# Performance work log

Measured on AMD Instinct MI355X. Metric: run time of the kernel, lower is better.

Reference implementation:

```python
import jax, jax.numpy as jnp
import numpy as np

RES = 32            # input grid resolution
OUT_RES = 64        # after subdivide
C = 128             # channels (== out_channels -> skip is identity)
G = 32              # group-norm groups
N = 8192            # active input voxels
EPS = 1e-5

# 8 child offsets for subdivide, 27 stencil offsets for 3x3x3 submanifold conv
_OFFS8 = np.stack(np.meshgrid([0, 1], [0, 1], [0, 1], indexing='ij'), -1).reshape(-1, 3).astype(np.int32)
_OFFS27 = np.stack(np.meshgrid([-1, 0, 1], [-1, 0, 1], [-1, 0, 1], indexing='ij'), -1).reshape(-1, 3).astype(np.int32)


def group_norm(x, gamma, beta, num_groups=G, eps=EPS):
    # sparse group norm over all active voxels of the (single) sample
    n, c = x.shape
    xg = x.reshape(n, num_groups, c // num_groups)
    mean = xg.mean(axis=(0, 2), keepdims=True)
    var = xg.var(axis=(0, 2), keepdims=True)
    xn = (xg - mean) * jax.lax.rsqrt(var + eps)
    return xn.reshape(n, c) * gamma + beta


def subdivide_coords(coords):
    offs = jnp.asarray(_OFFS8)
    return (coords[:, None, :] * 2 + offs[None, :, :]).reshape(-1, 3)  # [8N, 3]


def subm_conv3d(feats, coords, W, b, grid_res):
    # submanifold 3x3x3 sparse conv: outputs only at active sites
    n = feats.shape[0]
    grid = jnp.full((grid_res, grid_res, grid_res), -1, dtype=jnp.int32)
    grid = grid.at[coords[:, 0], coords[:, 1], coords[:, 2]].set(
        jnp.arange(n, dtype=jnp.int32))
    out = jnp.zeros((n, W.shape[-1]), dtype=feats.dtype)
    for k in range(27):  # fixed small stencil loop
        off = jnp.asarray(_OFFS27[k])
        nb = coords + off
        inb = jnp.all((nb >= 0) & (nb < grid_res), axis=1)
        nbc = jnp.clip(nb, 0, grid_res - 1)
        idx = grid[nbc[:, 0], nbc[:, 1], nbc[:, 2]]
        mask = inb & (idx >= 0)
        g = jnp.where(mask[:, None], feats[jnp.where(mask, idx, 0)], 0.0)
        out = out + g @ W[k]
    return out + b


def setup_inputs() -> dict:
    key = jax.random.key(0)
    ks = jax.random.split(key, 8)
    rng = np.random.default_rng(0)
    flat = rng.choice(RES ** 3, size=N, replace=False)
    coords = np.stack([flat // (RES * RES), (flat // RES) % RES, flat % RES],
                      axis=-1).astype(np.int32)
    feats = jax.random.normal(ks[0], (N, C), dtype=jnp.float32)
    gamma1 = 1.0 + 0.1 * jax.random.normal(ks[1], (C,), dtype=jnp.float32)
    beta1 = 0.1 * jax.random.normal(ks[2], (C,), dtype=jnp.float32)
    W1 = jax.random.normal(ks[3], (27, C, C), dtype=jnp.float32) * 0.05
    b1 = jax.random.normal(ks[4], (C,), dtype=jnp.float32) * 0.05
    gamma2 = 1.0 + 0.1 * jax.random.normal(ks[5], (C,), dtype=jnp.float32)
    beta2 = 0.1 * jax.random.normal(ks[6], (C,), dtype=jnp.float32)
    W2 = jax.random.normal(ks[7], (27, C, C), dtype=jnp.float32) * 0.05
    b2 = jax.random.normal(jax.random.fold_in(key, 99), (C,), dtype=jnp.float32) * 0.05
    return {"feats": feats, "gamma1": gamma1, "beta1": beta1, "W1": W1,
            "b1": b1, "gamma2": gamma2, "beta2": beta2, "W2": W2, "b2": b2,
            "coords": jnp.asarray(coords)}


def reference(feats, gamma1, beta1, W1, b1, gamma2, beta2, W2, b2, coords):
    # act_layers: GroupNorm + SiLU at input resolution
    h = jax.nn.silu(group_norm(feats, gamma1, beta1))
    # subdivide both branch and residual (8 children per voxel)
    new_coords = subdivide_coords(coords)          # [8N, 3] in OUT_RES grid
    h = jnp.repeat(h, 8, axis=0)
    x_sub = jnp.repeat(feats, 8, axis=0)
    # out_layers: conv3 -> GN -> SiLU -> conv3 (submanifold, same active set)
    h = subm_conv3d(h, new_coords, W1, b1, OUT_RES)
    h = jax.nn.silu(group_norm(h, gamma2, beta2))
    h = subm_conv3d(h, new_coords, W2, b2, OUT_RES)
    # skip_connection is Identity since out_channels == channels
    return h + x_sub
```

## Files before the change

### kernel.cpp

```cpp
#include <hip/hip_runtime.h>

#define NPAR   8192
#define NCH    65536
#define RES    32
#define EPS    1e-5f

typedef __attribute__((ext_vector_type(8))) short short8;
typedef __attribute__((ext_vector_type(4))) float floatx4;

__device__ __forceinline__ unsigned short f2bf(float f) {
    union { float f; unsigned u; } v; v.f = f;
    unsigned r = v.u + 0x7fffu + ((v.u >> 16) & 1u);
    return (unsigned short)(r >> 16);
}
__device__ __forceinline__ float bf2f(unsigned short b) {
    union { unsigned u; float f; } v; v.u = ((unsigned)b) << 16;
    return v.f;
}
__device__ __forceinline__ void glds16(const void* g, void* l) {
    __builtin_amdgcn_global_load_lds(
        (__attribute__((address_space(1))) const void*)g,
        (__attribute__((address_space(3))) void*)l, 16, 0, 0);
}
__device__ __forceinline__ int k27_of(int o, int s) {
    return (((o >> 2) & 1) + ((s >> 2) & 1)) * 9 +
           (((o >> 1) & 1) + ((s >> 1) & 1)) * 3 +
           ((o & 1) + (s & 1));
}
__device__ __forceinline__ void axis_dlist(int o, int s, int* d, int& n) {
    if (o == 0) { if (s == 0) { d[0] = -1; n = 1; } else { d[0] = 0; d[1] = 1; n = 2; } }
    else        { if (s == 0) { d[0] = -1; d[1] = 0; n = 2; } else { d[0] = 1; n = 1; } }
}

__global__ void k1_kernel(const int* __restrict__ coords, int* __restrict__ grid32,
                          const float* __restrict__ x, float* __restrict__ sum,
                          float* __restrict__ sq) {
    int b = blockIdx.x;
    int t = threadIdx.x;
    if (b < 32) {
        int p = b * 256 + t;
        grid32[(coords[p*3] << 10) + (coords[p*3+1] << 5) + coords[p*3+2]] = p;
    } else {
        __shared__ float s_sum[32], s_sq[32];
        if (t < 32) { s_sum[t] = 0.0f; s_sq[t] = 0.0f; }
        __syncthreads();
        const float4* x4 = (const float4*)x;
        int total = NPAR * 32;
        int idx0 = (b - 32) * 256 + t;
        int g = idx0 & 31;
        float ls = 0.0f, lq = 0.0f;
        for (int idx = idx0; idx < total; idx += 256 * 256) {
            float4 v = x4[idx];
            ls += v.x + v.y + v.z + v.w;
            lq += v.x * v.x + v.y * v.y + v.z * v.z + v.w * v.w;
        }
        atomicAdd(&s_sum[g], ls);
        atomicAdd(&s_sq[g], lq);
        __syncthreads();
        if (t < 32) { atomicAdd(&sum[t], s_sum[t]); atomicAdd(&sq[t], s_sq[t]); }
    }
}

__global__ void k2_kernel(const int* __restrict__ coords, const int* __restrict__ grid32,
                          int* __restrict__ idx_tab, int* __restrict__ pidx27,
                          const float* __restrict__ W1, const float* __restrict__ W2,
                          unsigned short* __restrict__ Wc1f, unsigned short* __restrict__ Wp2,
                          const float* __restrict__ x, const float* __restrict__ sum,
                          const float* __restrict__ sq, const float* __restrict__ gamma,
                          const float* __restrict__ beta, unsigned short* __restrict__ y) {
    int b = blockIdx.x;
    if (b < 256) {
        int R = b * 256 + threadIdx.x;
        int p = R >> 3, o = R & 7;
        int bx = 2 * coords[p*3]   + ((o >> 2) & 1);
        int by = 2 * coords[p*3+1] + ((o >> 1) & 1);
        int bz = 2 * coords[p*3+2] + (o & 1);
#pragma unroll 1
        for (int k = 0; k < 27; ++k) {
            int fx = bx + k / 9 - 1, fy = by + (k / 3) % 3 - 1, fz = bz + k % 3 - 1;
            int src = -1;
            if ((unsigned)fx < 64u && (unsigned)fy < 64u && (unsigned)fz < 64u) {
                int r = grid32[((fx >> 1) << 10) + ((fy >> 1) << 5) + (fz >> 1)];
                if ((unsigned)r < (unsigned)NPAR)
                    src = (((fx & 1) << 2) + ((fy & 1) << 1) + (fz & 1)) * NPAR + r;
            }
            idx_tab[k * NCH + R] = src;
        }
    } else if (b < 472) {
        int rem = (b - 256) * 256 + threadIdx.x;
        int lane = rem & 63;
        int ks   = (rem >> 6) & 3;
        int nb   = (rem >> 8) & 7;
        int tap  = rem >> 11;
        int n  = nb * 16 + (lane & 15);
        int k0 = ks * 32 + (lane >> 4) * 8;
        unsigned short v[8];
#pragma unroll
        for (int j = 0; j < 8; ++j) v[j] = f2bf(W2[tap * 16384 + (k0 + j) * 128 + n]);
        uint4 pk;
        pk.x = (unsigned)v[0] | ((unsigned)v[1] << 16);
        pk.y = (unsigned)v[2] | ((unsigned)v[3] << 16);
        pk.z = (unsigned)v[4] | ((unsigned)v[5] << 16);
        pk.w = (unsigned)v[6] | ((unsigned)v[7] << 16);
        *(uint4*)&Wp2[(long)rem * 8] = pk;
    } else if (b < 984) {
        int rem = (b - 472) * 256 + threadIdx.x;
        int lane  = rem & 63;
        int ks    = (rem >> 6) & 3;
        int nb    = (rem >> 8) & 7;
        int combo = rem >> 11;
        int o = combo >> 3, s = combo & 7;
        int n  = nb * 16 + (lane & 15);
        int k0 = ks * 32 + (lane >> 4) * 8;
        int d0[2], d1[2], d2[2], n0, n1, n2;
        axis_dlist((o >> 2) & 1, (s >> 2) & 1, d0, n0);
        axis_dlist((o >> 1) & 1, (s >> 1) & 1, d1, n1);
        axis_dlist(o & 1,        s & 1,        d2, n2);
        unsigned short v[8];
#pragma unroll
        for (int j = 0; j < 8; ++j) {
            float acc = 0.0f;
            for (int a = 0; a < n0; ++a)
                for (int bb = 0; bb < n1; ++bb)
                    for (int cc = 0; cc < n2; ++cc) {
                        int kk = (d0[a] + 1) * 9 + (d1[bb] + 1) * 3 + (d2[cc] + 1);
                        acc += W1[kk * 16384 + (k0 + j) * 128 + n];
                    }
            v[j] = f2bf(acc);
        }
        uint4 pk;
        pk.x = (unsigned)v[0] | ((unsigned)v[1] << 16);
        pk.y = (unsigned)v[2] | ((unsigned)v[3] << 16);
        pk.z = (unsigned)v[4] | ((unsigned)v[5] << 16);
        pk.w = (unsigned)v[6] | ((unsigned)v[7] << 16);
        *(uint4*)&Wc1f[(long)rem * 8] = pk;
    } else if (b < 1848) {
        int gid = (b - 984) * 256 + threadIdx.x;
        int k = gid >> 13, p = gid & 8191;
        int nx = coords[p*3]   + k / 9 - 1;
        int ny = coords[p*3+1] + (k / 3) % 3 - 1;
        int nz = coords[p*3+2] + k % 3 - 1;
        int src = -1;
        if ((unsigned)nx < 32u && (unsigned)ny < 32u && (unsigned)nz < 32u) {
            int r = grid32[(nx << 10) + (ny << 5) + nz];
            if ((unsigned)r < (unsigned)NPAR) src = r;
        }
        pidx27[k * NPAR + p] = src;
    } else {
        const float4* x4 = (const float4*)x;
        uint2* y2 = (uint2*)y;
        const float4* g4 = (const float4*)gamma;
        const float4* b4 = (const float4*)beta;
        float cnt = (float)NPAR * 4.0f;
        int total = NPAR * 32;
        for (int idx = (b - 1848) * 256 + threadIdx.x; idx < total; idx += 256 * 256) {
            int c4 = idx & 31;
            float mean = sum[c4] / cnt;
            float var = sq[c4] / cnt - mean * mean;
            float rstd = rsqrtf(var + EPS);
            float4 v = x4[idx];
            float4 gm = g4[c4];
            float4 bt = b4[c4];
            float a[4] = {v.x, v.y, v.z, v.w};
            float gg[4] = {gm.x, gm.y, gm.z, gm.w};
            float bb[4] = {bt.x, bt.y, bt.z, bt.w};
            unsigned short o[4];
#pragma unroll
            for (int i = 0; i < 4; ++i) {
                float tv = (a[i] - mean) * rstd * gg[i] + bb[i];
                o[i] = f2bf(tv / (1.0f + __expf(-tv)));
            }
            uint2 pk;
            pk.x = (unsigned)o[0] | ((unsigned)o[1] << 16);
            pk.y = (unsigned)o[2] | ((unsigned)o[3] << 16);
            y2[idx] = pk;
        }
    }
}

__global__ void gn_apply_bf16_kernel(unsigned short* __restrict__ x,
                                     const float* __restrict__ sum, const float* __restrict__ sq,
                                     const float* __restrict__ gamma, const float* __restrict__ beta,
                                     int nrows) {
    uint2* x2 = (uint2*)x;
    const float4* g4 = (const float4*)gamma;
    const float4* b4 = (const float4*)beta;
    float cnt = (float)nrows * 4.0f;
    int total = nrows * 32;
    for (int idx = blockIdx.x * blockDim.x + threadIdx.x; idx < total;
         idx += gridDim.x * blockDim.x) {
        int c4 = idx & 31;
        float mean = sum[c4] / cnt;
        float var = sq[c4] / cnt - mean * mean;
        float rstd = rsqrtf(var + EPS);
        uint2 pk = x2[idx];
        float a[4] = {bf2f((unsigned short)(pk.x & 0xffff)), bf2f((unsigned short)(pk.x >> 16)),
                      bf2f((unsigned short)(pk.y & 0xffff)), bf2f((unsigned short)(pk.y >> 16))};
        float4 gm = g4[c4];
        float4 bt = b4[c4];
        float gg[4] = {gm.x, gm.y, gm.z, gm.w};
        float bb[4] = {bt.x, bt.y, bt.z, bt.w};
        unsigned short o[4];
#pragma unroll
        for (int i = 0; i < 4; ++i) {
            float tv = (a[i] - mean) * rstd * gg[i] + bb[i];
            o[i] = f2bf(tv / (1.0f + __expf(-tv)));
        }
        pk.x = (unsigned)o[0] | ((unsigned)o[1] << 16);
        pk.y = (unsigned)o[2] | ((unsigned)o[3] << 16);
        x2[idx] = pk;
    }
}

__global__ void __launch_bounds__(256) conv1_fold_kernel(
    const unsigned short* __restrict__ Ag, const unsigned short* __restrict__ Wc1f,
    const float* __restrict__ bias, const int* __restrict__ pidx27,
    unsigned short* __restrict__ outp, const float* __restrict__ zpage,
    float* __restrict__ gsum, float* __restrict__ gsq) {
    __shared__ unsigned short A_lds[2][16384];

    int t = threadIdx.x;
    int o  = blockIdx.x & 7;
    int P0 = (blockIdx.x >> 3) << 7;
    const unsigned short* Wb = Wc1f + ((long)o << 17);
    int wv = t >> 6, lane = t & 63, quad = lane >> 4, l16 = lane & 15;
    int wm = wv & 1, wn = wv >> 1;
    int r16 = lane >> 2, cch = lane & 3;
    int c0 = wv * 2, c1 = wv * 2 + 1;
    int row0 = ((c0 >> 2) << 6) + ((c0 & 3) << 4) + r16;
    int row1 = ((c1 >> 2) << 6) + ((c1 & 3) << 4) + r16;
    int base0 = ((c0 >> 2) << 13) + ((c0 & 3) << 11);
    int base1 = ((c1 >> 2) << 13) + ((c1 & 3) << 11);
    const unsigned short* zsrc = (const unsigned short*)zpage;

    floatx4 acc[4][4];
#pragma unroll
    for (int mt = 0; mt < 4; ++mt)
#pragma unroll
        for (int nt = 0; nt < 4; ++nt)
            acc[mt][nt] = (floatx4){0.f, 0.f, 0.f, 0.f};

    int iv0 = pidx27[k27_of(o, 0) * NPAR + P0 + row0];
    int iv1 = pidx27[k27_of(o, 0) * NPAR + P0 + row1];
    {
        const unsigned short* g0 = (iv0 >= 0) ? Ag + (long)iv0 * 128 : zsrc;
        const unsigned short* g1 = (iv1 >= 0) ? Ag + (long)iv1 * 128 : zsrc;
#pragma unroll
        for (int i = 0; i < 4; ++i) glds16(g0 + i * 32 + cch * 8, &A_lds[0][base0 + i * 512]);
#pragma unroll
        for (int i = 0; i < 4; ++i) glds16(g1 + i * 32 + cch * 8, &A_lds[0][base1 + i * 512]);
    }
    int nv0 = pidx27[k27_of(o, 1) * NPAR + P0 + row0];
    int nv1 = pidx27[k27_of(o, 1) * NPAR + P0 + row1];
    __syncthreads();

#pragma unroll 1
    for (int s = 0; s < 8; ++s) {
        int cur = s & 1;
        if (s < 7) {
            const unsigned short* g0 = (nv0 >= 0) ? Ag + (long)nv0 * 128 : zsrc;
            const unsigned short* g1 = (nv1 >= 0) ? Ag + (long)nv1 * 128 : zsrc;
#pragma unroll
            for (int i = 0; i < 4; ++i) glds16(g0 + i * 32 + cch * 8, &A_lds[1 - cur][base0 + i * 512]);
#pragma unroll
            for (int i = 0; i < 4; ++i) glds16(g1 + i * 32 + cch * 8, &A_lds[1 - cur][base1 + i * 512]);
            if (s < 6) {
                nv0 = pidx27[k27_of(o, s + 2) * NPAR + P0 + row0];
                nv1 = pidx27[k27_of(o, s + 2) * NPAR + P0 + row1];
            }
        }
#pragma unroll
        for (int ks = 0; ks < 4; ++ks) {
            short8 afr[4], bfr[4];
#pragma unroll
            for (int mt = 0; mt < 4; ++mt)
                afr[mt] = *(const short8*)&A_lds[cur][(wm << 13) + (mt << 11) + (ks << 9) + (l16 << 5) + (quad << 3)];
#pragma unroll
            for (int nt = 0; nt < 4; ++nt) {
                int cb = wn * 4 + nt;
                bfr[nt] = *(const short8*)&Wb[((((s << 3) + cb) << 2) + ks) * 512 + (lane << 3)];
            }
#pragma unroll
            for (int mt = 0; mt < 4; ++mt)
#pragma unroll
                for (int nt = 0; nt < 4; ++nt)
                    acc[mt][nt] = __builtin_amdgcn_mfma_f32_16x16x32_bf16(
                        afr[mt], bfr[nt], acc[mt][nt], 0, 0, 0);
        }
        __syncthreads();
    }

    float s_[4] = {0.f, 0.f, 0.f, 0.f}, q_[4] = {0.f, 0.f, 0.f, 0.f};
#pragma unroll
    for (int nt = 0; nt < 4; ++nt) {
        int col = wn * 64 + nt * 16 + l16;
        float bv = bias[col];
#pragma unroll
        for (int mt = 0; mt < 4; ++mt) {
#pragma unroll
            for (int r = 0; r < 4; ++r) {
                int prow = wm * 64 + mt * 16 + quad * 4 + r;
                long R = (long)o * NPAR + P0 + prow;
                float v = acc[mt][nt][r] + bv;
                unsigned short u = f2bf(v);
                outp[R * 128 + col] = u;
                float vr = bf2f(u);
                s_[nt] += vr;
                q_[nt] += vr * vr;
            }
        }
    }
    float* sred = (float*)A_lds;
    if (t < 64) sred[t] = 0.0f;
    __syncthreads();
#pragma unroll
    for (int nt = 0; nt < 4; ++nt) {
        int g = (wn * 64 + nt * 16 + l16) >> 2;
        atomicAdd(&sred[g], s_[nt]);
        atomicAdd(&sred[32 + g], q_[nt]);
    }
    __syncthreads();
    if (t < 32) { atomicAdd(&gsum[t], sred[t]); atomicAdd(&gsq[t], sred[32 + t]); }
}

__global__ void __launch_bounds__(256) conv2_kernel(
    const unsigned short* __restrict__ Ag, const unsigned short* __restrict__ Wp,
    const float* __restrict__ bias, const int* __restrict__ idx_tab,
    const float* __restrict__ resid, float* __restrict__ outp,
    const float* __restrict__ zpage) {
    __shared__ unsigned short A_lds[2][16384];

    int t = threadIdx.x;
    int R0 = blockIdx.x * 128;
    int wv = t >> 6, lane = t & 63, quad = lane >> 4, l16 = lane & 15;
    int wm = wv & 1, wn = wv >> 1;
    int r16 = lane >> 2, cch = lane & 3;
    int c0 = wv * 2, c1 = wv * 2 + 1;
    int row0 = ((c0 >> 2) << 6) + ((c0 & 3) << 4) + r16;
    int row1 = ((c1 >> 2) << 6) + ((c1 & 3) << 4) + r16;
    int base0 = ((c0 >> 2) << 13) + ((c0 & 3) << 11);
    int base1 = ((c1 >> 2) << 13) + ((c1 & 3) << 11);
    const unsigned short* zsrc = (const unsigned short*)zpage;

    floatx4 acc[4][4];
#pragma unroll
    for (int mt = 0; mt < 4; ++mt)
#pragma unroll
        for (int nt = 0; nt < 4; ++nt)
            acc[mt][nt] = (floatx4){0.f, 0.f, 0.f, 0.f};

    int iv0 = idx_tab[R0 + row0], iv1 = idx_tab[R0 + row1];
    {
        const unsigned short* g0 = (iv0 >= 0) ? Ag + (long)iv0 * 128 : zsrc;
        const unsigned short* g1 = (iv1 >= 0) ? Ag + (long)iv1 * 128 : zsrc;
#pragma unroll
        for (int i = 0; i < 4; ++i) glds16(g0 + i * 32 + cch * 8, &A_lds[0][base0 + i * 512]);
#pragma unroll
        for (int i = 0; i < 4; ++i) glds16(g1 + i * 32 + cch * 8, &A_lds[0][base1 + i * 512]);
    }
    int nv0 = idx_tab[NCH + R0 + row0], nv1 = idx_tab[NCH + R0 + row1];
    __syncthreads();

#pragma unroll 1
    for (int k = 0; k < 27; ++k) {
        int cur = k & 1;
        if (k < 26) {
            const unsigned short* g0 = (nv0 >= 0) ? Ag + (long)nv0 * 128 : zsrc;
            const unsigned short* g1 = (nv1 >= 0) ? Ag + (long)nv1 * 128 : zsrc;
#pragma unroll
            for (int i = 0; i < 4; ++i) glds16(g0 + i * 32 + cch * 8, &A_lds[1 - cur][base0 + i * 512]);
#pragma unroll
            for (int i = 0; i < 4; ++i) glds16(g1 + i * 32 + cch * 8, &A_lds[1 - cur][base1 + i * 512]);
            if (k < 25) {
                nv0 = idx_tab[(k + 2) * NCH + R0 + row0];
                nv1 = idx_tab[(k + 2) * NCH + R0 + row1];
            }
        }
#pragma unroll
        for (int ks = 0; ks < 4; ++ks) {
            short8 afr[4], bfr[4];
#pragma unroll
            for (int mt = 0; mt < 4; ++mt)
                afr[mt] = *(const short8*)&A_lds[cur][(wm << 13) + (mt << 11) + (ks << 9) + (l16 << 5) + (quad << 3)];
#pragma unroll
            for (int nt = 0; nt < 4; ++nt) {
                int cb = wn * 4 + nt;
                bfr[nt] = *(const short8*)&Wp[((((k << 3) + cb) << 2) + ks) * 512 + (lane << 3)];
            }
#pragma unroll
            for (int mt = 0; mt < 4; ++mt)
#pragma unroll
                for (int nt = 0; nt < 4; ++nt)
                    acc[mt][nt] = __builtin_amdgcn_mfma_f32_16x16x32_bf16(
                        afr[mt], bfr[nt], acc[mt][nt], 0, 0, 0);
        }
        __syncthreads();
    }

#pragma unroll
    for (int nt = 0; nt < 4; ++nt) {
        int col = wn * 64 + nt * 16 + l16;
        float bv = bias[col];
#pragma unroll
        for (int mt = 0; mt < 4; ++mt) {
#pragma unroll
            for (int r = 0; r < 4; ++r) {
                int row = wm * 64 + mt * 16 + quad * 4 + r;
                long R = (long)R0 + row;
                float v = acc[mt][nt][r] + bv + resid[(R >> 3) * 128 + col];
                outp[R * 128 + col] = v;
            }
        }
    }
}

extern "C" void kernel_launch(void* const* d_in, const int* in_sizes, int n_in,
                              void* d_out, int out_size, void* d_ws, size_t ws_size,
                              hipStream_t stream) {
    const float* feats  = (const float*)d_in[0];
    const float* gamma1 = (const float*)d_in[1];
    const float* beta1  = (const float*)d_in[2];
    const float* W1     = (const float*)d_in[3];
    const float* b1     = (const float*)d_in[4];
    const float* gamma2 = (const float*)d_in[5];
    const float* beta2  = (const float*)d_in[6];
    const float* W2     = (const float*)d_in[7];
    const float* b2     = (const float*)d_in[8];
    const int*   coords = (const int*)d_in[9];
    float* out = (float*)d_out;

    char* ws = (char*)d_ws;
    unsigned short* h0b  = (unsigned short*)(ws);
    unsigned short* h1b  = (unsigned short*)(ws + (2u << 20));
    unsigned short* Wc1f = (unsigned short*)(ws + (18u << 20));
    unsigned short* Wp2  = (unsigned short*)(ws + (20u << 20));
    int*   grid32        = (int*)  (ws + (21u << 20));
    float* stats         = (float*)(ws + (21u << 20) + 131072);
    float* zpage         = (float*)(ws + (21u << 20) + 131072 + 512);
    int*   idx_tab       = (int*)  (ws + (22u << 20));
    int*   pidx27        = (int*)  (ws + (30u << 20));

    hipMemsetAsync(stats, 0, 1024, stream);

    k1_kernel<<<288, 256, 0, stream>>>(coords, grid32, feats, stats + 0, stats + 32);
    k2_kernel<<<2104, 256, 0, stream>>>(coords, grid32, idx_tab, pidx27,
                                        W1, W2, Wc1f, Wp2,
                                        feats, stats + 0, stats + 32, gamma1, beta1, h0b);

    conv1_fold_kernel<<<8 * (NPAR / 128), 256, 0, stream>>>(h0b, Wc1f, b1, pidx27,
                                                            h1b, zpage,
                                                            stats + 64, stats + 96);

    gn_apply_bf16_kernel<<<512, 256, 0, stream>>>(h1b, stats + 64, stats + 96, gamma2, beta2, NCH);

    conv2_kernel<<<NCH / 128, 256, 0, stream>>>(h1b, Wp2, b2, idx_tab,
                                                feats, out, zpage);
}
```

Baseline: 211.7 us.

## Prefetch weight fragments into registers one tap ahead in conv kernels

Both conv kernels now load the B (weight) fragments for the next stencil tap into a second register set while MFMAs run on the current tap. This mirrors the existing double-buffered LDS staging of gathered activations, so global weight loads no longer sit directly in front of the MFMA chain. The loop is unrolled by two with ping-pong register buffers, and launch_bounds gains a minimum of 2 blocks per SM, which caps registers. The group-norm apply kernel grid is also doubled. Holding two 16-entry short8 weight arrays adds register pressure, and the occupancy hint could cause spills.

```diff
diff --git a/kernel.cpp b/kernel.cpp
--- a/kernel.cpp
+++ b/kernel.cpp
@@ -212,7 +212,44 @@
     }
 }
 
-__global__ void __launch_bounds__(256) conv1_fold_kernel(
+__device__ __forceinline__ void mfma_phase(
+    const unsigned short* __restrict__ Abuf, short8 (&bfr)[4][4],
+    floatx4 (&acc)[4][4], int wm, int l16, int quad) {
+#pragma unroll
+    for (int ks = 0; ks < 4; ++ks) {
+        short8 afr[4];
+#pragma unroll
+        for (int mt = 0; mt < 4; ++mt)
+            afr[mt] = *(const short8*)&Abuf[(wm << 13) + (mt << 11) + (ks << 9) + (l16 << 5) + (quad << 3)];
+#pragma unroll
+        for (int mt = 0; mt < 4; ++mt)
+#pragma unroll
+            for (int nt = 0; nt < 4; ++nt)
+                acc[mt][nt] = __builtin_amdgcn_mfma_f32_16x16x32_bf16(
+                    afr[mt], bfr[nt][ks], acc[mt][nt], 0, 0, 0);
+    }
+}
+__device__ __forceinline__ void loadB(const unsigned short* __restrict__ Wtap,
+                                      short8 (&bfr)[4][4], int wn, int lane) {
+#pragma unroll
+    for (int nt = 0; nt < 4; ++nt)
+#pragma unroll
+        for (int ks = 0; ks < 4; ++ks)
+            bfr[nt][ks] = *(const short8*)&Wtap[(((wn * 4 + nt) << 2) + ks) * 512 + (lane << 3)];
+}
+__device__ __forceinline__ void stageA(const unsigned short* __restrict__ Ag,
+                                       int iv0, int iv1, const unsigned short* zsrc,
+                                       unsigned short* __restrict__ buf,
+                                       int base0, int base1, int cch) {
+    const unsigned short* g0 = (iv0 >= 0) ? Ag + (long)iv0 * 128 : zsrc;
+    const unsigned short* g1 = (iv1 >= 0) ? Ag + (long)iv1 * 128 : zsrc;
+#pragma unroll
+    for (int i = 0; i < 4; ++i) glds16(g0 + i * 32 + cch * 8, &buf[base0 + i * 512]);
+#pragma unroll
+    for (int i = 0; i < 4; ++i) glds16(g1 + i * 32 + cch * 8, &buf[base1 + i * 512]);
+}
+
+__global__ void __launch_bounds__(256, 2) conv1_fold_kernel(
     const unsigned short* __restrict__ Ag, const unsigned short* __restrict__ Wc1f,
     const float* __restrict__ bias, const int* __restrict__ pidx27,
     unsigned short* __restrict__ outp, const float* __restrict__ zpage,
@@ -239,54 +276,34 @@
 #pragma unroll
         for (int nt = 0; nt < 4; ++nt)
             acc[mt][nt] = (floatx4){0.f, 0.f, 0.f, 0.f};
-
-    int iv0 = pidx27[k27_of(o, 0) * NPAR + P0 + row0];
-    int iv1 = pidx27[k27_of(o, 0) * NPAR + P0 + row1];
-    {
-        const unsigned short* g0 = (iv0 >= 0) ? Ag + (long)iv0 * 128 : zsrc;
-        const unsigned short* g1 = (iv1 >= 0) ? Ag + (long)iv1 * 128 : zsrc;
-#pragma unroll
-        for (int i = 0; i < 4; ++i) glds16(g0 + i * 32 + cch * 8, &A_lds[0][base0 + i * 512]);
-#pragma unroll
-        for (int i = 0; i < 4; ++i) glds16(g1 + i * 32 + cch * 8, &A_lds[0][base1 + i * 512]);
-    }
+    short8 bA[4][4], bB[4][4];
+
+    stageA(Ag, pidx27[k27_of(o, 0) * NPAR + P0 + row0],
+               pidx27[k27_of(o, 0) * NPAR + P0 + row1], zsrc, A_lds[0], base0, base1, cch);
+    loadB(Wb, bA, wn, lane);
     int nv0 = pidx27[k27_of(o, 1) * NPAR + P0 + row0];
     int nv1 = pidx27[k27_of(o, 1) * NPAR + P0 + row1];
     __syncthreads();
 
 #pragma unroll 1
-    for (int s = 0; s < 8; ++s) {
-        int cur = s & 1;
-        if (s < 7) {
-            const unsigned short* g0 = (nv0 >= 0) ? Ag + (long)nv0 * 128 : zsrc;
-            const unsigned short* g1 = (nv1 >= 0) ? Ag + (long)nv1 * 128 : zsrc;
-#pragma unroll
-            for (int i = 0; i < 4; ++i) glds16(g0 + i * 32 + cch * 8, &A_lds[1 - cur][base0 + i * 512]);
-#pragma unroll
-            for (int i = 0; i < 4; ++i) glds16(g1 + i * 32 + cch * 8, &A_lds[1 - cur][base1 + i * 512]);
-            if (s < 6) {
-                nv0 = pidx27[k27_of(o, s + 2) * NPAR + P0 + row0];
-                nv1 = pidx27[k27_of(o, s + 2) * NPAR + P0 + row1];
-            }
-        }
-#pragma unroll
-        for (int ks = 0; ks < 4; ++ks) {
-            short8 afr[4], bfr[4];
-#pragma unroll
-            for (int mt = 0; mt < 4; ++mt)
-                afr[mt] = *(const short8*)&A_lds[cur][(wm << 13) + (mt << 11) + (ks << 9) + (l16 << 5) + (quad << 3)];
-#pragma unroll
-            for (int nt = 0; nt < 4; ++nt) {
-                int cb = wn * 4 + nt;
-                bfr[nt] = *(const short8*)&Wb[((((s << 3) + cb) << 2) + ks) * 512 + (lane << 3)];
-            }
-#pragma unroll
-            for (int mt = 0; mt < 4; ++mt)
-#pragma unroll
-                for (int nt = 0; nt < 4; ++nt)
-                    acc[mt][nt] = __builtin_amdgcn_mfma_f32_16x16x32_bf16(
-                        afr[mt], bfr[nt], acc[mt][nt], 0, 0, 0);
-        }
+    for (int s = 0; s < 8; s += 2) {
+        stageA(Ag, nv0, nv1, zsrc, A_lds[1], base0, base1, cch);
+        loadB(Wb + ((long)(s + 1) << 14), bB, wn, lane);
+        if (s + 2 < 8) {
+            nv0 = pidx27[k27_of(o, s + 2) * NPAR + P0 + row0];
+            nv1 = pidx27[k27_of(o, s + 2) * NPAR + P0 + row1];
+        }
+        mfma_phase(A_lds[0], bA, acc, wm, l16, quad);
+        __syncthreads();
+        if (s + 2 < 8) {
+            stageA(Ag, nv0, nv1, zsrc, A_lds[0], base0, base1, cch);
+            loadB(Wb + ((long)(s + 2) << 14), bA, wn, lane);
+            if (s + 3 < 8) {
+                nv0 = pidx27[k27_of(o, s + 3) * NPAR + P0 + row0];
+                nv1 = pidx27[k27_of(o, s + 3) * NPAR + P0 + row1];
+            }
+        }
+        mfma_phase(A_lds[1], bB, acc, wm, l16, quad);
         __syncthreads();
     }
 
@@ -323,7 +340,7 @@
     if (t < 32) { atomicAdd(&gsum[t], sred[t]); atomicAdd(&gsq[t], sred[32 + t]); }
 }
 
-__global__ void __launch_bounds__(256) conv2_kernel(
+__global__ void __launch_bounds__(256, 2) conv2_kernel(
     const unsigned short* __restrict__ Ag, const unsigned short* __restrict__ Wp,
     const float* __restrict__ bias, const int* __restrict__ idx_tab,
     const float* __restrict__ resid, float* __restrict__ outp,
@@ -348,53 +365,37 @@
 #pragma unroll
         for (int nt = 0; nt < 4; ++nt)
             acc[mt][nt] = (floatx4){0.f, 0.f, 0.f, 0.f};
-
-    int iv0 = idx_tab[R0 + row0], iv1 = idx_tab[R0 + row1];
-    {
-        const unsigned short* g0 = (iv0 >= 0) ? Ag + (long)iv0 * 128 : zsrc;
-        const unsigned short* g1 = (iv1 >= 0) ? Ag + (long)iv1 * 128 : zsrc;
-#pragma unroll
-        for (int i = 0; i < 4; ++i) glds16(g0 + i * 32 + cch * 8, &A_lds[0][base0 + i * 512]);
-#pragma unroll
-        for (int i = 0; i < 4; ++i) glds16(g1 + i * 32 + cch * 8, &A_lds[0][base1 + i * 512]);
-    }
+    short8 bA[4][4], bB[4][4];
+
+    stageA(Ag, idx_tab[R0 + row0], idx_tab[R0 + row1], zsrc, A_lds[0], base0, base1, cch);
+    loadB(Wp, bA, wn, lane);
     int nv0 = idx_tab[NCH + R0 + row0], nv1 = idx_tab[NCH + R0 + row1];
     __syncthreads();
 
 #pragma unroll 1
-    for (int k = 0; k < 27; ++k) {
-        int cur = k & 1;
-        if (k < 26) {
-            const unsigned short* g0 = (nv0 >= 0) ? Ag + (long)nv0 * 128 : zsrc;
-            const unsigned short* g1 = (nv1 >= 0) ? Ag + (long)nv1 * 128 : zsrc;
-#pragma unroll
-            for (int i = 0; i < 4; ++i) glds16(g0 + i * 32 + cch * 8, &A_lds[1 - cur][base0 + i * 512]);
-#pragma unroll
-            for (int i = 0; i < 4; ++i) glds16(g1 + i * 32 + cch * 8, &A_lds[1 - cur][base1 + i * 512]);
-            if (k < 25) {
+    for (int k = 0; k < 27; k += 2) {
+        if (k + 1 < 27) {
+            stageA(Ag, nv0, nv1, zsrc, A_lds[1], base0, base1, cch);
+            loadB(Wp + ((long)(k + 1) << 14), bB, wn, lane);
+            if (k + 2 < 27) {
                 nv0 = idx_tab[(k + 2) * NCH + R0 + row0];
                 nv1 = idx_tab[(k + 2) * NCH + R0 + row1];
             }
         }
-#pragma unroll
-        for (int ks = 0; ks < 4; ++ks) {
-            short8 afr[4], bfr[4];
-#pragma unroll
-            for (int mt = 0; mt < 4; ++mt)
-                afr[mt] = *(const short8*)&A_lds[cur][(wm << 13) + (mt << 11) + (ks << 9) + (l16 << 5) + (quad << 3)];
-#pragma unroll
-            for (int nt = 0; nt < 4; ++nt) {
-                int cb = wn * 4 + nt;
-                bfr[nt] = *(const short8*)&Wp[((((k << 3) + cb) << 2) + ks) * 512 + (lane << 3)];
-            }
-#pragma unroll
-            for (int mt = 0; mt < 4; ++mt)
-#pragma unroll
-                for (int nt = 0; nt < 4; ++nt)
-                    acc[mt][nt] = __builtin_amdgcn_mfma_f32_16x16x32_bf16(
-                        afr[mt], bfr[nt], acc[mt][nt], 0, 0, 0);
-        }
+        mfma_phase(A_lds[0], bA, acc, wm, l16, quad);
         __syncthreads();
+        if (k + 1 < 27) {
+            if (k + 2 < 27) {
+                stageA(Ag, nv0, nv1, zsrc, A_lds[0], base0, base1, cch);
+                loadB(Wp + ((long)(k + 2) << 14), bA, wn, lane);
+                if (k + 3 < 27) {
+                    nv0 = idx_tab[(k + 3) * NCH + R0 + row0];
+                    nv1 = idx_tab[(k + 3) * NCH + R0 + row1];
+                }
+            }
+            mfma_phase(A_lds[1], bB, acc, wm, l16, quad);
+            __syncthreads();
+        }
     }
 
 #pragma unroll
@@ -451,7 +452,7 @@
                                                             h1b, zpage,
                                                             stats + 64, stats + 96);
 
-    gn_apply_bf16_kernel<<<512, 256, 0, stream>>>(h1b, stats + 64, stats + 96, gamma2, beta2, NCH);
+    gn_apply_bf16_kernel<<<1024, 256, 0, stream>>>(h1b, stats + 64, stats + 96, gamma2, beta2, NCH);
 
     conv2_kernel<<<NCH / 128, 256, 0, stream>>>(h1b, Wp2, b2, idx_tab,
                                                 feats, out, zpage);
```

Measured after the change: 205.7 us. 2.9% less time.
